# Optimization experiments

Measured on AMD Instinct MI355X. Metric: run time of the kernel, lower is better.

## Reference

```python
import jax, jax.numpy as jnp
import numpy as np

D_IN = 128
D_OUT = 128
B, N = 8, 2048
NEG = -9e15


def setup_inputs() -> dict:
    key = jax.random.key(0)
    ks = jax.random.split(key, 7)
    x = jax.random.normal(ks[0], (B, N, D_IN), dtype=jnp.float32)
    adj = jax.random.randint(ks[1], (B, N, N), 0, 2).astype(jnp.float32)
    s_in = 1.0 / np.sqrt(D_IN)
    s_out = 1.0 / np.sqrt(D_OUT)
    s_g = 1.0 / np.sqrt(2 * D_OUT)
    # torch.nn.Linear weights stored pre-transposed: [in, out]
    W_w = jax.random.uniform(ks[2], (D_IN, D_OUT), jnp.float32, -s_in, s_in)
    W_b = jax.random.uniform(ks[3], (D_OUT,), jnp.float32, -s_in, s_in)
    A_w = jax.random.uniform(ks[4], (D_OUT, D_OUT), jnp.float32, -s_out, s_out)
    gate_w = jax.random.uniform(ks[5], (2 * D_OUT, 1), jnp.float32, -s_g, s_g)
    gate_b = jax.random.uniform(ks[6], (1,), jnp.float32, -s_g, s_g)
    return {"x": x, "adj": adj, "W_w": W_w, "W_b": W_b, "A_w": A_w,
            "gate_w": gate_w, "gate_b": gate_b}


def reference(x, adj, W_w, W_b, A_w, gate_w, gate_b):
    h = x @ W_w + W_b                                  # [B,N,D]
    e = jnp.einsum('bnd,bmd->bnm', h @ A_w, h)          # [B,N,N]
    e = e + jnp.swapaxes(e, 1, 2)                       # symmetric
    att = jnp.where(adj > 0, e, NEG)
    att = jax.nn.softmax(att, axis=1)                   # NOTE: dim=1 as in torch code
    att = att * adj
    h_prime = jax.nn.relu(jnp.einsum('bnm,bmd->bnd', att, h))
    coeff = jax.nn.sigmoid(jnp.concatenate([x, h_prime], axis=-1) @ gate_w + gate_b)  # [B,N,1]
    return coeff * x + (1.0 - coeff) * h_prime
```

## Files before the change

kernel.cpp:

```cpp
#include <hip/hip_runtime.h>
#include <hip/hip_bf16.h>

#define B_ 8
#define N_ 2048
#define D_ 128

typedef __bf16 bf16_t;
typedef __bf16 v8bf __attribute__((ext_vector_type(8)));
typedef float  v4f  __attribute__((ext_vector_type(4)));

__global__ __launch_bounds__(256) void k_prep(
    const float* __restrict__ Ww, const float* __restrict__ Aw,
    bf16_t* __restrict__ WT, bf16_t* __restrict__ AT)
{
    int idx = blockIdx.x * 256 + threadIdx.x;
    int o = idx >> 7, i = idx & 127;
    WT[idx] = (bf16_t)Ww[i * D_ + o];
    AT[idx] = (bf16_t)Aw[i * D_ + o];
}

__global__ __launch_bounds__(256) void k_hg(
    const float* __restrict__ x, const float* __restrict__ Wb,
    const bf16_t* __restrict__ WT, const bf16_t* __restrict__ AT,
    bf16_t* __restrict__ hb, bf16_t* __restrict__ gb)
{
    int wave = threadIdx.x >> 6;
    int lane = threadIdx.x & 63;
    int q = lane >> 4;
    int c = lane & 15;
    int nrow0 = blockIdx.x * 64 + wave * 16;

    __shared__ float pw_all[4][16][132];
    float (*pw)[132] = pw_all[wave];

    v8bf ax[4];
#pragma unroll
    for (int kc = 0; kc < 4; ++kc) {
        const float* src = x + (size_t)(nrow0 + c) * D_ + kc * 32 + q * 8;
        float4 f0 = *(const float4*)src;
        float4 f1 = *(const float4*)(src + 4);
        v8bf a;
        a[0]=(bf16_t)f0.x; a[1]=(bf16_t)f0.y; a[2]=(bf16_t)f0.z; a[3]=(bf16_t)f0.w;
        a[4]=(bf16_t)f1.x; a[5]=(bf16_t)f1.y; a[6]=(bf16_t)f1.z; a[7]=(bf16_t)f1.w;
        ax[kc] = a;
    }

#pragma unroll
    for (int ct = 0; ct < 8; ++ct) {
        float bias = Wb[ct * 16 + c];
        v4f acc = {bias, bias, bias, bias};
#pragma unroll
        for (int kc = 0; kc < 4; ++kc) {
            v8bf bw = *(const v8bf*)(WT + (size_t)(ct * 16 + c) * D_ + kc * 32 + q * 8);
            acc = __builtin_amdgcn_mfma_f32_16x16x32_bf16(ax[kc], bw, acc, 0, 0, 0);
        }
#pragma unroll
        for (int r = 0; r < 4; ++r) pw[q * 4 + r][ct * 16 + c] = acc[r];
    }
    __builtin_amdgcn_wave_barrier();

    v8bf ahf[4];
#pragma unroll
    for (int kc = 0; kc < 4; ++kc) {
        v4f p0 = *(const v4f*)&pw[c][kc * 32 + q * 8];
        v4f p1 = *(const v4f*)&pw[c][kc * 32 + q * 8 + 4];
        v8bf a;
#pragma unroll
        for (int j = 0; j < 4; ++j) { a[j] = (bf16_t)p0[j]; a[j+4] = (bf16_t)p1[j]; }
        ahf[kc] = a;
    }
    {
        int row = lane >> 2, seg = lane & 3;
#pragma unroll
        for (int v = 0; v < 4; ++v) {
            v8bf hv;
#pragma unroll
            for (int j = 0; j < 8; ++j) hv[j] = (bf16_t)pw[row][seg * 32 + v * 8 + j];
            *(v8bf*)(hb + (size_t)(nrow0 + row) * D_ + seg * 32 + v * 8) = hv;
        }
    }
    __builtin_amdgcn_wave_barrier();

#pragma unroll
    for (int ct = 0; ct < 8; ++ct) {
        v4f acc = {0.f, 0.f, 0.f, 0.f};
#pragma unroll
        for (int kc = 0; kc < 4; ++kc) {
            v8bf bw = *(const v8bf*)(AT + (size_t)(ct * 16 + c) * D_ + kc * 32 + q * 8);
            acc = __builtin_amdgcn_mfma_f32_16x16x32_bf16(ahf[kc], bw, acc, 0, 0, 0);
        }
#pragma unroll
        for (int r = 0; r < 4; ++r) pw[q * 4 + r][ct * 16 + c] = acc[r];
    }
    __builtin_amdgcn_wave_barrier();
    {
        int row = lane >> 2, seg = lane & 3;
#pragma unroll
        for (int v = 0; v < 4; ++v) {
            v8bf gv;
#pragma unroll
            for (int j = 0; j < 8; ++j) gv[j] = (bf16_t)pw[row][seg * 32 + v * 8 + j];
            *(v8bf*)(gb + (size_t)(nrow0 + row) * D_ + seg * 32 + v * 8) = gv;
        }
    }
}

__global__ __launch_bounds__(256, 2) void k_att(
    const bf16_t* __restrict__ hb, const bf16_t* __restrict__ gb,
    const float* __restrict__ adj, float* __restrict__ colsum,
    bf16_t* __restrict__ Pt)
{
    int bid = blockIdx.x;
    int b = bid & 7;
    int rest = bid >> 3;
    int nblk = rest >> 3;
    int mgrp = rest & 7;
    int wave = threadIdx.x >> 6;
    int lane = threadIdx.x & 63;
    int q = lane >> 4;
    int c = lane & 15;
    int nbase = nblk * 64;
    int mwav = mgrp * 256 + wave * 64;
    const size_t hgoff = (size_t)b * N_ * D_;
    const float* adjb = adj + (size_t)b * N_ * N_;

    __shared__ float eb_all[4][64][68];
    float (*eb)[68] = eb_all[wave];

    v8bf ag[4][4], ah[4][4];
#pragma unroll
    for (int sub = 0; sub < 4; ++sub)
#pragma unroll
        for (int kc = 0; kc < 4; ++kc) {
            size_t off = hgoff + (size_t)(nbase + sub * 16 + c) * D_ + kc * 32 + q * 8;
            ag[sub][kc] = *(const v8bf*)(gb + off);
            ah[sub][kc] = *(const v8bf*)(hb + off);
        }

    for (int t = 0; t < 4; ++t) {
        int mt = mwav + t * 16;
        float av[4][4];
#pragma unroll
        for (int sub = 0; sub < 4; ++sub)
#pragma unroll
            for (int r = 0; r < 4; ++r)
                av[sub][r] = adjb[(size_t)(nbase + sub * 16 + q * 4 + r) * N_ + mt + c];
        v8bf bh[4], bg[4];
#pragma unroll
        for (int kc = 0; kc < 4; ++kc) {
            size_t off = hgoff + (size_t)(mt + c) * D_ + kc * 32 + q * 8;
            bh[kc] = *(const v8bf*)(hb + off);
            bg[kc] = *(const v8bf*)(gb + off);
        }
        v4f e[4];
#pragma unroll
        for (int sub = 0; sub < 4; ++sub) e[sub] = (v4f){0.f, 0.f, 0.f, 0.f};
#pragma unroll
        for (int kc = 0; kc < 4; ++kc)
#pragma unroll
            for (int sub = 0; sub < 4; ++sub) {
                e[sub] = __builtin_amdgcn_mfma_f32_16x16x32_bf16(ag[sub][kc], bh[kc], e[sub], 0, 0, 0);
                e[sub] = __builtin_amdgcn_mfma_f32_16x16x32_bf16(ah[sub][kc], bg[kc], e[sub], 0, 0, 0);
            }
        float cs = 0.f;
#pragma unroll
        for (int sub = 0; sub < 4; ++sub)
#pragma unroll
            for (int r = 0; r < 4; ++r) {
                float ex = __expf(e[sub][r]);
                float pv = (av[sub][r] > 0.f) ? ex : 0.f;
                eb[sub * 16 + q * 4 + r][t * 16 + c] = pv;
                cs += pv;
            }
        cs += __shfl_xor(cs, 16);
        cs += __shfl_xor(cs, 32);
        if (lane < 16) atomicAdd(&colsum[b * N_ + mt + lane], cs);
    }
    __builtin_amdgcn_wave_barrier();
    int prow = lane >> 3, pseg = lane & 7;
#pragma unroll
    for (int pass = 0; pass < 8; ++pass) {
        int row = pass * 8 + prow;
        v4f p0 = *(const v4f*)&eb[row][pseg * 8];
        v4f p1 = *(const v4f*)&eb[row][pseg * 8 + 4];
        v8bf o;
#pragma unroll
        for (int j = 0; j < 4; ++j) { o[j] = (bf16_t)p0[j]; o[j + 4] = (bf16_t)p1[j]; }
        *(v8bf*)(Pt + ((size_t)b * N_ + nbase + row) * N_ + mwav + pseg * 8) = o;
    }
}

__global__ __launch_bounds__(256) void k_scaleT(
    const bf16_t* __restrict__ hb, const float* __restrict__ colsum,
    bf16_t* __restrict__ hbTs)
{
    int bid = blockIdx.x;
    int b = bid >> 6;
    int rem = bid & 63;
    int nblk = rem >> 1;
    int dblk = rem & 1;
    int tid = threadIdx.x;
    __shared__ bf16_t sm[64][72];
    __shared__ float sinv[64];
    int n0 = nblk * 64, d0 = dblk * 64;
    int r = tid >> 3, cg = tid & 7;
#pragma unroll
    for (int rr = 0; rr < 2; ++rr) {
        int row = r + rr * 32;
        *(v8bf*)&sm[row][cg * 8] =
            *(const v8bf*)(hb + (size_t)(b * N_ + n0 + row) * D_ + d0 + cg * 8);
    }
    if (tid < 64) {
        float s = colsum[b * N_ + n0 + tid];
        sinv[tid] = (s > 0.f) ? 1.f / s : 0.f;
    }
    __syncthreads();
#pragma unroll
    for (int rr = 0; rr < 2; ++rr) {
        int dr = r + rr * 32;
        v8bf v;
#pragma unroll
        for (int jj = 0; jj < 8; ++jj)
            v[jj] = (bf16_t)((float)sm[cg * 8 + jj][dr] * sinv[cg * 8 + jj]);
        *(v8bf*)(hbTs + (size_t)(b * D_ + d0 + dr) * N_ + n0 + cg * 8) = v;
    }
}

__global__ __launch_bounds__(512, 2) void k_out(
    const bf16_t* __restrict__ Pt, const bf16_t* __restrict__ hbTs,
    const float* __restrict__ x, const float* __restrict__ gw,
    const float* __restrict__ gbias, float* __restrict__ out)
{
    int bid = blockIdx.x;
    int b = bid & 7;
    int nblk = bid >> 3;
    int tid = threadIdx.x;
    int wave = tid >> 6;
    int lane = tid & 63;
    int q = lane >> 4;
    int c = lane & 15;
    int nbase = nblk * 64;
    int m0 = wave * 256;

    __shared__ float hp[64][132];

    const bf16_t* hTb = hbTs + (size_t)b * D_ * N_;
    const bf16_t* Pb  = Pt + (size_t)b * N_ * N_;

    v4f acc[4][8];
#pragma unroll
    for (int sub = 0; sub < 4; ++sub)
#pragma unroll
        for (int dt = 0; dt < 8; ++dt) acc[sub][dt] = (v4f){0.f, 0.f, 0.f, 0.f};

    for (int ch = 0; ch < 8; ++ch) {
        int mch = m0 + ch * 32;
        v8bf a[4];
#pragma unroll
        for (int sub = 0; sub < 4; ++sub)
            a[sub] = *(const v8bf*)(Pb + (size_t)(nbase + sub * 16 + c) * N_ + mch + q * 8);
        v8bf vt[8];
#pragma unroll
        for (int dt = 0; dt < 8; ++dt)
            vt[dt] = *(const v8bf*)(hTb + (size_t)(dt * 16 + c) * N_ + mch + q * 8);
#pragma unroll
        for (int dt = 0; dt < 8; ++dt)
#pragma unroll
            for (int sub = 0; sub < 4; ++sub)
                acc[sub][dt] = __builtin_amdgcn_mfma_f32_16x16x32_bf16(a[sub], vt[dt], acc[sub][dt], 0, 0, 0);
    }

    if (wave == 0) {
#pragma unroll
        for (int sub = 0; sub < 4; ++sub)
#pragma unroll
            for (int dt = 0; dt < 8; ++dt)
#pragma unroll
                for (int r = 0; r < 4; ++r)
                    hp[sub * 16 + q * 4 + r][dt * 16 + c] = acc[sub][dt][r];
    }
    __syncthreads();
#pragma unroll
    for (int wv = 1; wv < 8; ++wv) {
        if (wave == wv) {
#pragma unroll
            for (int sub = 0; sub < 4; ++sub)
#pragma unroll
                for (int dt = 0; dt < 8; ++dt)
#pragma unroll
                    for (int r = 0; r < 4; ++r)
                        hp[sub * 16 + q * 4 + r][dt * 16 + c] += acc[sub][dt][r];
        }
        __syncthreads();
    }

    int row = tid >> 3;
    int seg = tid & 7;
    size_t g = (size_t)b * N_ + nbase + row;
    const float* xr = x + g * D_ + seg * 16;
    float xv[16], hv[16];
#pragma unroll
    for (int j = 0; j < 16; j += 4) {
        float4 f = *(const float4*)(xr + j);
        xv[j] = f.x; xv[j+1] = f.y; xv[j+2] = f.z; xv[j+3] = f.w;
    }
#pragma unroll
    for (int j = 0; j < 16; ++j) hv[j] = fmaxf(hp[row][seg * 16 + j], 0.f);
    float part = 0.f;
#pragma unroll
    for (int j = 0; j < 16; ++j)
        part += xv[j] * gw[seg * 16 + j] + hv[j] * gw[D_ + seg * 16 + j];
    part += __shfl_xor(part, 1);
    part += __shfl_xor(part, 2);
    part += __shfl_xor(part, 4);
    float coeff = 1.f / (1.f + __expf(-(part + gbias[0])));
    float* orow = out + g * D_ + seg * 16;
#pragma unroll
    for (int j = 0; j < 16; j += 4) {
        float4 o;
        o.x = coeff * xv[j]   + (1.f - coeff) * hv[j];
        o.y = coeff * xv[j+1] + (1.f - coeff) * hv[j+1];
        o.z = coeff * xv[j+2] + (1.f - coeff) * hv[j+2];
        o.w = coeff * xv[j+3] + (1.f - coeff) * hv[j+3];
        *(float4*)(orow + j) = o;
    }
}

extern "C" void kernel_launch(void* const* d_in, const int* in_sizes, int n_in,
                              void* d_out, int out_size, void* d_ws, size_t ws_size,
                              hipStream_t stream)
{
    const float* x     = (const float*)d_in[0];
    const float* adj   = (const float*)d_in[1];
    const float* Ww    = (const float*)d_in[2];
    const float* Wb    = (const float*)d_in[3];
    const float* Aw    = (const float*)d_in[4];
    const float* gw    = (const float*)d_in[5];
    const float* gbias = (const float*)d_in[6];
    float* out = (float*)d_out;

    char* ws = (char*)d_ws;
    bf16_t* hb     = (bf16_t*)(ws);
    bf16_t* gb     = (bf16_t*)(ws + (4 << 20));
    bf16_t* hbTs   = (bf16_t*)(ws + (8 << 20));
    float*  colsum = (float*)(ws + (12 << 20));
    bf16_t* Pt     = (bf16_t*)(ws + (17 << 20));
    bf16_t* WT     = (bf16_t*)(ws + (81 << 20));
    bf16_t* AT     = (bf16_t*)(ws + (81 << 20) + (32 << 10));

    hipMemsetAsync(colsum, 0, B_ * N_ * sizeof(float), stream);
    k_prep<<<64, 256, 0, stream>>>(Ww, Aw, WT, AT);
    k_hg<<<B_ * N_ / 64, 256, 0, stream>>>(x, Wb, WT, AT, hb, gb);
    k_att<<<2048, 256, 0, stream>>>(hb, gb, adj, colsum, Pt);
    k_scaleT<<<512, 256, 0, stream>>>(hb, colsum, hbTs);
    k_out<<<256, 512, 0, stream>>>(Pt, hbTs, x, gw, gbias, out);
}
```

Measured before the change: 316.3 us.

## Retile attention and output kernels, drop LDS staging and cross-wave reduction

k_att now processes 32 query rows per block across 512 columns, writes P directly to global as scalar bf16 stores instead of staging through LDS, splits the MFMA accumulation into two independent chains, and raises the occupancy hint to 3. k_out changes from splitting the reduction dimension across waves, which needed a serialized shared-memory sum, to splitting rows and D across waves so each wave owns its output tile. The aim is to cut LDS use and barriers and to raise occupancy. In exchange, k_att's stores become scattered 2-byte writes and k_out waves each reload the P rows along the full reduction length.

New measurement: 423.1 us. +33.7%, slower.

```diff
diff --git a/kernel.cpp b/kernel.cpp
--- a/kernel.cpp
+++ b/kernel.cpp
@@ -105,7 +105,7 @@
     }
 }
 
-__global__ __launch_bounds__(256, 2) void k_att(
+__global__ __launch_bounds__(256, 3) void k_att(
     const bf16_t* __restrict__ hb, const bf16_t* __restrict__ gb,
     const float* __restrict__ adj, float* __restrict__ colsum,
     bf16_t* __restrict__ Pt)
@@ -113,23 +113,21 @@
     int bid = blockIdx.x;
     int b = bid & 7;
     int rest = bid >> 3;
-    int nblk = rest >> 3;
-    int mgrp = rest & 7;
+    int nblk = rest >> 2;
+    int mgrp = rest & 3;
     int wave = threadIdx.x >> 6;
     int lane = threadIdx.x & 63;
     int q = lane >> 4;
     int c = lane & 15;
-    int nbase = nblk * 64;
-    int mwav = mgrp * 256 + wave * 64;
+    int nbase = nblk * 32;
+    int mwav = mgrp * 512 + wave * 128;
     const size_t hgoff = (size_t)b * N_ * D_;
     const float* adjb = adj + (size_t)b * N_ * N_;
-
-    __shared__ float eb_all[4][64][68];
-    float (*eb)[68] = eb_all[wave];
-
-    v8bf ag[4][4], ah[4][4];
-#pragma unroll
-    for (int sub = 0; sub < 4; ++sub)
+    bf16_t* Pb = Pt + (size_t)b * N_ * N_;
+
+    v8bf ag[2][4], ah[2][4];
+#pragma unroll
+    for (int sub = 0; sub < 2; ++sub)
 #pragma unroll
         for (int kc = 0; kc < 4; ++kc) {
             size_t off = hgoff + (size_t)(nbase + sub * 16 + c) * D_ + kc * 32 + q * 8;
@@ -137,11 +135,11 @@
             ah[sub][kc] = *(const v8bf*)(hb + off);
         }
 
-    for (int t = 0; t < 4; ++t) {
+    for (int t = 0; t < 8; ++t) {
         int mt = mwav + t * 16;
-        float av[4][4];
-#pragma unroll
-        for (int sub = 0; sub < 4; ++sub)
+        float av[2][4];
+#pragma unroll
+        for (int sub = 0; sub < 2; ++sub)
 #pragma unroll
             for (int r = 0; r < 4; ++r)
                 av[sub][r] = adjb[(size_t)(nbase + sub * 16 + q * 4 + r) * N_ + mt + c];
@@ -152,41 +150,33 @@
             bh[kc] = *(const v8bf*)(hb + off);
             bg[kc] = *(const v8bf*)(gb + off);
         }
-        v4f e[4];
-#pragma unroll
-        for (int sub = 0; sub < 4; ++sub) e[sub] = (v4f){0.f, 0.f, 0.f, 0.f};
+        v4f e0[2], e1[2];
+#pragma unroll
+        for (int sub = 0; sub < 2; ++sub) {
+            e0[sub] = (v4f){0.f, 0.f, 0.f, 0.f};
+            e1[sub] = (v4f){0.f, 0.f, 0.f, 0.f};
+        }
 #pragma unroll
         for (int kc = 0; kc < 4; ++kc)
 #pragma unroll
-            for (int sub = 0; sub < 4; ++sub) {
-                e[sub] = __builtin_amdgcn_mfma_f32_16x16x32_bf16(ag[sub][kc], bh[kc], e[sub], 0, 0, 0);
-                e[sub] = __builtin_amdgcn_mfma_f32_16x16x32_bf16(ah[sub][kc], bg[kc], e[sub], 0, 0, 0);
+            for (int sub = 0; sub < 2; ++sub) {
+                e0[sub] = __builtin_amdgcn_mfma_f32_16x16x32_bf16(ag[sub][kc], bh[kc], e0[sub], 0, 0, 0);
+                e1[sub] = __builtin_amdgcn_mfma_f32_16x16x32_bf16(ah[sub][kc], bg[kc], e1[sub], 0, 0, 0);
             }
         float cs = 0.f;
 #pragma unroll
-        for (int sub = 0; sub < 4; ++sub)
+        for (int sub = 0; sub < 2; ++sub)
 #pragma unroll
             for (int r = 0; r < 4; ++r) {
-                float ex = __expf(e[sub][r]);
+                float ev = e0[sub][r] + e1[sub][r];
+                float ex = __expf(ev);
                 float pv = (av[sub][r] > 0.f) ? ex : 0.f;
-                eb[sub * 16 + q * 4 + r][t * 16 + c] = pv;
                 cs += pv;
+                Pb[(size_t)(nbase + sub * 16 + q * 4 + r) * N_ + mt + c] = (bf16_t)pv;
             }
         cs += __shfl_xor(cs, 16);
         cs += __shfl_xor(cs, 32);
         if (lane < 16) atomicAdd(&colsum[b * N_ + mt + lane], cs);
-    }
-    __builtin_amdgcn_wave_barrier();
-    int prow = lane >> 3, pseg = lane & 7;
-#pragma unroll
-    for (int pass = 0; pass < 8; ++pass) {
-        int row = pass * 8 + prow;
-        v4f p0 = *(const v4f*)&eb[row][pseg * 8];
-        v4f p1 = *(const v4f*)&eb[row][pseg * 8 + 4];
-        v8bf o;
-#pragma unroll
-        for (int j = 0; j < 4; ++j) { o[j] = (bf16_t)p0[j]; o[j + 4] = (bf16_t)p1[j]; }
-        *(v8bf*)(Pt + ((size_t)b * N_ + nbase + row) * N_ + mwav + pseg * 8) = o;
     }
 }
 
@@ -240,59 +230,37 @@
     int q = lane >> 4;
     int c = lane & 15;
     int nbase = nblk * 64;
-    int m0 = wave * 256;
+    int nsub = wave & 3;
+    int dhalf = wave >> 2;
 
     __shared__ float hp[64][132];
 
     const bf16_t* hTb = hbTs + (size_t)b * D_ * N_;
     const bf16_t* Pb  = Pt + (size_t)b * N_ * N_;
-
-    v4f acc[4][8];
-#pragma unroll
-    for (int sub = 0; sub < 4; ++sub)
-#pragma unroll
-        for (int dt = 0; dt < 8; ++dt) acc[sub][dt] = (v4f){0.f, 0.f, 0.f, 0.f};
-
-    for (int ch = 0; ch < 8; ++ch) {
-        int mch = m0 + ch * 32;
-        v8bf a[4];
-#pragma unroll
-        for (int sub = 0; sub < 4; ++sub)
-            a[sub] = *(const v8bf*)(Pb + (size_t)(nbase + sub * 16 + c) * N_ + mch + q * 8);
-        v8bf vt[8];
-#pragma unroll
-        for (int dt = 0; dt < 8; ++dt)
-            vt[dt] = *(const v8bf*)(hTb + (size_t)(dt * 16 + c) * N_ + mch + q * 8);
-#pragma unroll
-        for (int dt = 0; dt < 8; ++dt)
-#pragma unroll
-            for (int sub = 0; sub < 4; ++sub)
-                acc[sub][dt] = __builtin_amdgcn_mfma_f32_16x16x32_bf16(a[sub], vt[dt], acc[sub][dt], 0, 0, 0);
-    }
-
-    if (wave == 0) {
-#pragma unroll
-        for (int sub = 0; sub < 4; ++sub)
-#pragma unroll
-            for (int dt = 0; dt < 8; ++dt)
-#pragma unroll
-                for (int r = 0; r < 4; ++r)
-                    hp[sub * 16 + q * 4 + r][dt * 16 + c] = acc[sub][dt][r];
-    }
+    const bf16_t* Arow = Pb + (size_t)(nbase + nsub * 16 + c) * N_;
+
+    v4f acc[4];
+#pragma unroll
+    for (int dt = 0; dt < 4; ++dt) acc[dt] = (v4f){0.f, 0.f, 0.f, 0.f};
+
+    for (int ch = 0; ch < 64; ++ch) {
+        int mch = ch * 32;
+        v8bf a = *(const v8bf*)(Arow + mch + q * 8);
+        v8bf vt[4];
+#pragma unroll
+        for (int dt = 0; dt < 4; ++dt)
+            vt[dt] = *(const v8bf*)(hTb + (size_t)(dhalf * 64 + dt * 16 + c) * N_ + mch + q * 8);
+#pragma unroll
+        for (int dt = 0; dt < 4; ++dt)
+            acc[dt] = __builtin_amdgcn_mfma_f32_16x16x32_bf16(a, vt[dt], acc[dt], 0, 0, 0);
+    }
+
+#pragma unroll
+    for (int dt = 0; dt < 4; ++dt)
+#pragma unroll
+        for (int r = 0; r < 4; ++r)
+            hp[nsub * 16 + q * 4 + r][dhalf * 64 + dt * 16 + c] = acc[dt][r];
     __syncthreads();
-#pragma unroll
-    for (int wv = 1; wv < 8; ++wv) {
-        if (wave == wv) {
-#pragma unroll
-            for (int sub = 0; sub < 4; ++sub)
-#pragma unroll
-                for (int dt = 0; dt < 8; ++dt)
-#pragma unroll
-                    for (int r = 0; r < 4; ++r)
-                        hp[sub * 16 + q * 4 + r][dt * 16 + c] += acc[sub][dt][r];
-        }
-        __syncthreads();
-    }
 
     int row = tid >> 3;
     int seg = tid & 7;
```
